# Optimization experiments

Measured on AMD Instinct MI355X. Metric: run time of the kernel, lower is better.

Reference implementation:

```python
import jax, jax.numpy as jnp
import numpy as np

TEMPERATURE = 8.0  # sqrt(d) with d = 64


def setup_inputs() -> dict:
    key = jax.random.key(0)
    kq, kk, kv, kmq, kmk = jax.random.split(key, 5)
    b, n, m, d, dv = 8, 4096, 4096, 64, 64
    return {
        "queries": jax.random.normal(kq, (b, n, d), dtype=jnp.float32),
        "keys": jax.random.normal(kk, (b, m, d), dtype=jnp.float32),
        "values": jax.random.normal(kv, (b, m, dv), dtype=jnp.float32),
        "mask_query": jax.random.randint(kmq, (b, n), 0, 2, dtype=jnp.int32),
        "mask_key": jax.random.randint(kmk, (b, m), 0, 2, dtype=jnp.int32),
    }


def reference(queries, keys, values, mask_query, mask_key):
    # scores: [b, n, m]
    attention = jnp.einsum("bnd,bmd->bnm", queries, keys)
    # multiplicative query mask: [b, n] -> [b, n, 1]
    attention = attention * mask_query[:, :, None].astype(queries.dtype)
    # additive log key mask: [b, m] -> [b, 1, m]; log(0) = -inf masks keys out
    attention = attention + jnp.log(mask_key[:, None, :].astype(queries.dtype))
    attention = jax.nn.softmax(attention / TEMPERATURE, axis=2)
    # output: [b, n, d']
    return jnp.einsum("bnm,bmv->bnv", attention, values)
```

## Files before the change

### kernel.cpp

```cpp
#include <hip/hip_runtime.h>


#define B_ 8
#define N_ 4096
#define M_ 4096
#define D_ 64

typedef __attribute__((ext_vector_type(8))) __bf16 bfrag;
typedef __attribute__((ext_vector_type(16))) float f32x16;
typedef __attribute__((ext_vector_type(4))) float f32x4;

union FragU { bfrag f; unsigned int u[4]; };

__device__ __forceinline__ unsigned int pkbf(float lo, float hi) {
  unsigned short a = __builtin_bit_cast(unsigned short, (__bf16)lo);
  unsigned short b = __builtin_bit_cast(unsigned short, (__bf16)hi);
  return ((unsigned int)b << 16) | (unsigned int)a;
}
__device__ __forceinline__ unsigned short bf1(float x) {
  return __builtin_bit_cast(unsigned short, (__bf16)x);
}

__global__ void attn_prepass(const float* __restrict__ kg, const float* __restrict__ vg,
                             char* __restrict__ kpack, char* __restrict__ vpack)
{
  const int bid = blockIdx.x, tid = threadIdx.x;
  if (bid < 1024) {
    const unsigned c0 = bid * 256 + tid;
    const int lane = c0 & 63;
    const unsigned u = c0 >> 6;
    const int f = u & 1, c = (u >> 1) & 3, tile = (u >> 3) & 63, batch = u >> 9;
    const int lq = lane & 31, lh = lane >> 5;
    const int row = tile * 64 + f * 32 + lq;
    const float* src = kg + (((size_t)batch * M_ + row) * D_ + c * 16 + lh * 8);
    float4 a = ((const float4*)src)[0], b = ((const float4*)src)[1];
    uint4 o;
    o.x = pkbf(a.x, a.y); o.y = pkbf(a.z, a.w);
    o.z = pkbf(b.x, b.y); o.w = pkbf(b.z, b.w);
    *(uint4*)(kpack + (size_t)c0 * 16) = o;
  } else {
    const unsigned c0 = (bid - 1024) * 256 + tid;
    const int lane = c0 & 63;
    const unsigned u = c0 >> 6;
    const int f = u & 1, mc = (u >> 1) & 3, tile = (u >> 3) & 63, batch = u >> 9;
    const int lq = lane & 31, lh = lane >> 5;
    const int key0 = tile * 64 + mc * 16 + lh * 8;
    const int dv = f * 32 + lq;
    const float* base = vg + (((size_t)batch * M_ + key0) * D_ + dv);
    unsigned short h[8];
#pragma unroll
    for (int j = 0; j < 8; ++j) h[j] = bf1(base[(size_t)j * D_]);
    uint4 o;
    o.x = (unsigned)h[0] | ((unsigned)h[1] << 16);
    o.y = (unsigned)h[2] | ((unsigned)h[3] << 16);
    o.z = (unsigned)h[4] | ((unsigned)h[5] << 16);
    o.w = (unsigned)h[6] | ((unsigned)h[7] << 16);
    *(uint4*)(vpack + (size_t)c0 * 16) = o;
  }
}

__global__ __launch_bounds__(256, 2) void attn_main(
    const float* __restrict__ qg, const int* __restrict__ mqg,
    const int* __restrict__ mkg, const char* __restrict__ kpack,
    const char* __restrict__ vpack, float* __restrict__ outg)
{
  __shared__ alignas(16) char smem[34048];
  const int tid  = threadIdx.x;
  const int lane = tid & 63;
  const int lq   = lane & 31;
  const int lh   = lane >> 5;
  const int wid  = tid >> 6;
  const int batch = blockIdx.x & 7;
  const int qbase = (blockIdx.x >> 3) * 64;

  float* lArrA = (float*)(smem + 32768);
  float* lArrB = (float*)(smem + 33280);
  float* IlvA  = (float*)(smem + 33792);
  float* IlvB  = (float*)(smem + 33920);

  {
    const int4* mk4 = (const int4*)(mkg + batch * M_);
    float* bl = (float*)smem;
#pragma unroll
    for (int j = 0; j < 4; ++j) {
      const int i4 = tid + j * 256;
      int4 m4 = mk4[i4];
      f32x4 bv;
      bv[0] = m4.x ? 0.f : -1e30f;
      bv[1] = m4.y ? 0.f : -1e30f;
      bv[2] = m4.z ? 0.f : -1e30f;
      bv[3] = m4.w ? 0.f : -1e30f;
      *(f32x4*)(bl + i4 * 4) = bv;
    }
  }

  bfrag qfA[4], qfB[4];
  {
    const int growA = qbase + lq;
    const float qsA = mqg[batch * N_ + growA] ? 0.1803368801111204f : 0.0f;
    const float* QpA = qg + ((size_t)batch * N_ + growA) * D_ + lh * 8;
#pragma unroll
    for (int c = 0; c < 4; ++c) {
      float4 a = *(const float4*)(QpA + c * 16);
      float4 b = *(const float4*)(QpA + c * 16 + 4);
      FragU f;
      f.u[0] = pkbf(a.x * qsA, a.y * qsA);
      f.u[1] = pkbf(a.z * qsA, a.w * qsA);
      f.u[2] = pkbf(b.x * qsA, b.y * qsA);
      f.u[3] = pkbf(b.z * qsA, b.w * qsA);
      qfA[c] = f.f;
    }
    const int growB = qbase + 32 + lq;
    const float qsB = mqg[batch * N_ + growB] ? 0.1803368801111204f : 0.0f;
    const float* QpB = qg + ((size_t)batch * N_ + growB) * D_ + lh * 8;
#pragma unroll
    for (int c = 0; c < 4; ++c) {
      float4 a = *(const float4*)(QpB + c * 16);
      float4 b = *(const float4*)(QpB + c * 16 + 4);
      FragU f;
      f.u[0] = pkbf(a.x * qsB, a.y * qsB);
      f.u[1] = pkbf(a.z * qsB, a.w * qsB);
      f.u[2] = pkbf(b.x * qsB, b.y * qsB);
      f.u[3] = pkbf(b.z * qsB, b.w * qsB);
      qfB[c] = f.f;
    }
  }
  __syncthreads();

  f32x16 oA0, oA1, oB0, oB1;
#pragma unroll
  for (int i = 0; i < 16; ++i) { oA0[i] = 0.f; oA1[i] = 0.f; oB0[i] = 0.f; oB1[i] = 0.f; }
  float lsumA = 0.f, lsumB = 0.f;

  const float* blw = (const float*)smem + wid * 1024;

  for (int t16 = 0; t16 < 16; ++t16) {
    const int tile = wid * 16 + t16;
    const size_t tb = (size_t)(batch * 64 + tile) * 8192 + (size_t)lane * 16;

    bfrag kf[4][2];
#pragma unroll
    for (int c = 0; c < 4; ++c) {
      kf[c][0] = *(const bfrag*)(kpack + tb + (c * 2 + 0) * 1024);
      kf[c][1] = *(const bfrag*)(kpack + tb + (c * 2 + 1) * 1024);
    }
    bfrag vf[4][2];
#pragma unroll
    for (int mc = 0; mc < 4; ++mc) {
      vf[mc][0] = *(const bfrag*)(vpack + tb + (mc * 2 + 0) * 1024);
      vf[mc][1] = *(const bfrag*)(vpack + tb + (mc * 2 + 1) * 1024);
    }

    f32x16 sA0, sA1, sB0, sB1;
#pragma unroll
    for (int i = 0; i < 16; ++i) { sA0[i] = 0.f; sA1[i] = 0.f; sB0[i] = 0.f; sB1[i] = 0.f; }
    __builtin_amdgcn_s_setprio(1);
#pragma unroll
    for (int c = 0; c < 4; ++c) {
      sA0 = __builtin_amdgcn_mfma_f32_32x32x16_bf16(kf[c][0], qfA[c], sA0, 0, 0, 0);
      sA1 = __builtin_amdgcn_mfma_f32_32x32x16_bf16(kf[c][1], qfA[c], sA1, 0, 0, 0);
      sB0 = __builtin_amdgcn_mfma_f32_32x32x16_bf16(kf[c][0], qfB[c], sB0, 0, 0, 0);
      sB1 = __builtin_amdgcn_mfma_f32_32x32x16_bf16(kf[c][1], qfB[c], sB1, 0, 0, 0);
    }
    __builtin_amdgcn_s_setprio(0);

    const float* bb = blw + t16 * 64;
    f32x4 psvA = {0.f, 0.f, 0.f, 0.f}, psvB = {0.f, 0.f, 0.f, 0.f};
#pragma unroll
    for (int g = 0; g < 4; ++g) {
      f32x4 b0 = *(const f32x4*)(bb + g * 8 + 4 * lh);
      f32x4 b1 = *(const f32x4*)(bb + 32 + g * 8 + 4 * lh);
#pragma unroll
      for (int r = 0; r < 4; ++r) {
        float pA0 = __builtin_amdgcn_exp2f(sA0[g * 4 + r] + b0[r]);
        float pA1 = __builtin_amdgcn_exp2f(sA1[g * 4 + r] + b1[r]);
        float pB0 = __builtin_amdgcn_exp2f(sB0[g * 4 + r] + b0[r]);
        float pB1 = __builtin_amdgcn_exp2f(sB1[g * 4 + r] + b1[r]);
        sA0[g * 4 + r] = pA0; sA1[g * 4 + r] = pA1;
        sB0[g * 4 + r] = pB0; sB1[g * 4 + r] = pB1;
        psvA[r] += pA0 + pA1;
        psvB[r] += pB0 + pB1;
      }
    }
    float psA = (psvA[0] + psvA[1]) + (psvA[2] + psvA[3]);
    float psB = (psvB[0] + psvB[1]) + (psvB[2] + psvB[3]);
    psA += __shfl_xor(psA, 32);
    psB += __shfl_xor(psB, 32);
    lsumA += psA;
    lsumB += psB;

#pragma unroll
    for (int mc = 0; mc < 4; ++mc) {
      unsigned int c01, c23, c45, c67;
      {
        const int Rb = (mc & 1) * 8;
        if (mc < 2) {
          c01 = pkbf(sA0[Rb + 0], sA0[Rb + 1]); c23 = pkbf(sA0[Rb + 2], sA0[Rb + 3]);
          c45 = pkbf(sA0[Rb + 4], sA0[Rb + 5]); c67 = pkbf(sA0[Rb + 6], sA0[Rb + 7]);
        } else {
          c01 = pkbf(sA1[Rb + 0], sA1[Rb + 1]); c23 = pkbf(sA1[Rb + 2], sA1[Rb + 3]);
          c45 = pkbf(sA1[Rb + 4], sA1[Rb + 5]); c67 = pkbf(sA1[Rb + 6], sA1[Rb + 7]);
        }
      }
      unsigned int t01 = (unsigned int)__shfl_xor((int)c01, 32);
      unsigned int t23 = (unsigned int)__shfl_xor((int)c23, 32);
      unsigned int t45 = (unsigned int)__shfl_xor((int)c45, 32);
      unsigned int t67 = (unsigned int)__shfl_xor((int)c67, 32);
      FragU pa;
      pa.u[0] = lh ? t45 : c01;
      pa.u[1] = lh ? t67 : c23;
      pa.u[2] = lh ? c45 : t01;
      pa.u[3] = lh ? c67 : t23;
      __builtin_amdgcn_s_setprio(1);
      oA0 = __builtin_amdgcn_mfma_f32_32x32x16_bf16(pa.f, vf[mc][0], oA0, 0, 0, 0);
      oA1 = __builtin_amdgcn_mfma_f32_32x32x16_bf16(pa.f, vf[mc][1], oA1, 0, 0, 0);
      __builtin_amdgcn_s_setprio(0);
    }
#pragma unroll
    for (int mc = 0; mc < 4; ++mc) {
      unsigned int c01, c23, c45, c67;
      {
        const int Rb = (mc & 1) * 8;
        if (mc < 2) {
          c01 = pkbf(sB0[Rb + 0], sB0[Rb + 1]); c23 = pkbf(sB0[Rb + 2], sB0[Rb + 3]);
          c45 = pkbf(sB0[Rb + 4], sB0[Rb + 5]); c67 = pkbf(sB0[Rb + 6], sB0[Rb + 7]);
        } else {
          c01 = pkbf(sB1[Rb + 0], sB1[Rb + 1]); c23 = pkbf(sB1[Rb + 2], sB1[Rb + 3]);
          c45 = pkbf(sB1[Rb + 4], sB1[Rb + 5]); c67 = pkbf(sB1[Rb + 6], sB1[Rb + 7]);
        }
      }
      unsigned int t01 = (unsigned int)__shfl_xor((int)c01, 32);
      unsigned int t23 = (unsigned int)__shfl_xor((int)c23, 32);
      unsigned int t45 = (unsigned int)__shfl_xor((int)c45, 32);
      unsigned int t67 = (unsigned int)__shfl_xor((int)c67, 32);
      FragU pa;
      pa.u[0] = lh ? t45 : c01;
      pa.u[1] = lh ? t67 : c23;
      pa.u[2] = lh ? c45 : t01;
      pa.u[3] = lh ? c67 : t23;
      __builtin_amdgcn_s_setprio(1);
      oB0 = __builtin_amdgcn_mfma_f32_32x32x16_bf16(pa.f, vf[mc][0], oB0, 0, 0, 0);
      oB1 = __builtin_amdgcn_mfma_f32_32x32x16_bf16(pa.f, vf[mc][1], oB1, 0, 0, 0);
      __builtin_amdgcn_s_setprio(0);
    }
  }

  if (lane < 32) { lArrA[wid * 32 + lane] = lsumA; lArrB[wid * 32 + lane] = lsumB; }
  __syncthreads();
  {
    float ltA = 0.f, ltB = 0.f;
#pragma unroll
    for (int w = 0; w < 4; ++w) { ltA += lArrA[w * 32 + lq]; ltB += lArrB[w * 32 + lq]; }
    if (wid == 0 && lane < 32) { IlvA[lane] = 1.f / ltA; IlvB[lane] = 1.f / ltB; }
  }
  __syncthreads();
#pragma unroll
  for (int g = 0; g < 4; ++g) {
    f32x4 IvA = *(const f32x4*)(IlvA + g * 8 + 4 * lh);
    f32x4 IvB = *(const f32x4*)(IlvB + g * 8 + 4 * lh);
#pragma unroll
    for (int rr = 0; rr < 4; ++rr) {
      oA0[g * 4 + rr] *= IvA[rr];
      oA1[g * 4 + rr] *= IvA[rr];
      oB0[g * 4 + rr] *= IvB[rr];
      oB1[g * 4 + rr] *= IvB[rr];
    }
  }
  float* bufsA = (float*)smem;
  float* bufsB = (float*)smem + 4096;
  float* dA = bufsA + (wid & 1) * 2048;
  float* dB = bufsB + (wid & 1) * 2048;
  if (wid < 2) {
#pragma unroll
    for (int r = 0; r < 16; ++r) {
      const int row = (r & 3) + 8 * (r >> 2) + 4 * lh;
      dA[row * 64 + lq]      = oA0[r];
      dA[row * 64 + 32 + lq] = oA1[r];
      dB[row * 64 + lq]      = oB0[r];
      dB[row * 64 + 32 + lq] = oB1[r];
    }
  }
  __syncthreads();
  if (wid >= 2) {
#pragma unroll
    for (int r = 0; r < 16; ++r) {
      const int row = (r & 3) + 8 * (r >> 2) + 4 * lh;
      dA[row * 64 + lq]      += oA0[r];
      dA[row * 64 + 32 + lq] += oA1[r];
      dB[row * 64 + lq]      += oB0[r];
      dB[row * 64 + 32 + lq] += oB1[r];
    }
  }
  __syncthreads();
  {
    float* op = outg + ((size_t)batch * N_ + qbase) * 64;
    const int i = tid * 8;
    f32x4 a0 = *(const f32x4*)(bufsA + i),     a1 = *(const f32x4*)(bufsA + 2048 + i);
    f32x4 b0 = *(const f32x4*)(bufsA + i + 4), b1 = *(const f32x4*)(bufsA + 2048 + i + 4);
#pragma unroll
    for (int r = 0; r < 4; ++r) { a0[r] += a1[r]; b0[r] += b1[r]; }
    *(f32x4*)(op + i)     = a0;
    *(f32x4*)(op + i + 4) = b0;
    f32x4 c0 = *(const f32x4*)(bufsB + i),     c1 = *(const f32x4*)(bufsB + 2048 + i);
    f32x4 d0 = *(const f32x4*)(bufsB + i + 4), d1 = *(const f32x4*)(bufsB + 2048 + i + 4);
#pragma unroll
    for (int r = 0; r < 4; ++r) { c0[r] += c1[r]; d0[r] += d1[r]; }
    *(f32x4*)(op + 2048 + i)     = c0;
    *(f32x4*)(op + 2048 + i + 4) = d0;
  }
}

__device__ __forceinline__ unsigned int swz(unsigned int byte) {
  return byte ^ (((byte >> 7) & 7) << 4);
}

__global__ __launch_bounds__(256, 2) void attn_fused(
    const float* __restrict__ qg, const float* __restrict__ kg,
    const float* __restrict__ vg, const int* __restrict__ mqg,
    const int* __restrict__ mkg, float* __restrict__ outg)
{
  __shared__ alignas(16) char smem[35072];
  const int tid  = threadIdx.x;
  const int lane = tid & 63;
  const int lq   = lane & 31;
  const int lh   = lane >> 5;
  const int wid  = tid >> 6;
  const int khalf = wid >> 1;
  const int qrw  = (wid & 1) * 32;
  const int batch = blockIdx.x & 7;
  const int qbase = (blockIdx.x >> 3) * 64;

  char* Kl = smem + khalf * 8192;
  char* Vl = smem + 16384 + khalf * 8192;
  float* kbf    = (float*)(smem + 32768);
  float* alphav = (float*)(smem + 33280);
  float* mM     = (float*)(smem + 33792);
  float* mL     = (float*)(smem + 34048);
  float* bC0    = (float*)(smem + 34304);
  float* bC1    = (float*)(smem + 34560);

  const int grow = qbase + qrw + lq;
  const float qs = mqg[batch * N_ + grow] ? 0.1803368801111204f : 0.0f;
  bfrag qf[4];
  {
    const float* Qp = qg + ((size_t)batch * N_ + grow) * D_ + lh * 8;
#pragma unroll
    for (int c = 0; c < 4; ++c) {
      float4 a = *(const float4*)(Qp + c * 16);
      float4 b = *(const float4*)(Qp + c * 16 + 4);
      FragU f;
      f.u[0] = pkbf(a.x * qs, a.y * qs);
      f.u[1] = pkbf(a.z * qs, a.w * qs);
      f.u[2] = pkbf(b.x * qs, b.y * qs);
      f.u[3] = pkbf(b.z * qs, b.w * qs);
      qf[c] = f.f;
    }
  }

  const int sid   = tid & 127;
  const int shalf = tid >> 7;

  f32x16 o0, o1;
#pragma unroll
  for (int i = 0; i < 16; ++i) { o0[i] = 0.f; o1[i] = 0.f; }
  float m2 = -1e30f, lsum = 0.f;

  for (int t = 0; t < 32; ++t) {
    __syncthreads();
    {
      const int kb0 = shalf * 2048 + t * 64;
      const float4* K4 = (const float4*)(kg + ((size_t)batch * M_ + kb0) * D_);
      const float4* V4 = (const float4*)(vg + ((size_t)batch * M_ + kb0) * D_);
      char* Ks = smem + shalf * 8192;
      char* Vs = smem + 16384 + shalf * 8192;
#pragma unroll
      for (int j = 0; j < 8; ++j) {
        int idx = sid + j * 128;
        float4 a = K4[idx];
        int row = idx >> 4, col = (idx & 15) << 2;
        *(uint2*)(Ks + swz((unsigned)(row * 128 + col * 2))) =
            make_uint2(pkbf(a.x, a.y), pkbf(a.z, a.w));
        float4 b = V4[idx];
        int vk = idx >> 4, vc = (idx & 15) << 2;
        *(unsigned short*)(Vs + swz((unsigned)((vc + 0) * 128 + vk * 2))) = bf1(b.x);
        *(unsigned short*)(Vs + swz((unsigned)((vc + 1) * 128 + vk * 2))) = bf1(b.y);
        *(unsigned short*)(Vs + swz((unsigned)((vc + 2) * 128 + vk * 2))) = bf1(b.z);
        *(unsigned short*)(Vs + swz((unsigned)((vc + 3) * 128 + vk * 2))) = bf1(b.w);
      }
      if (sid < 64)
        kbf[shalf * 64 + sid] = mkg[batch * M_ + kb0 + sid] ? 0.f : -1e30f;
    }
    __syncthreads();

    f32x16 s0, s1;
#pragma unroll
    for (int i = 0; i < 16; ++i) { s0[i] = 0.f; s1[i] = 0.f; }
#pragma unroll
    for (int c = 0; c < 4; ++c) {
      bfrag kf0 = *(const bfrag*)(Kl + swz((unsigned)(lq * 128 + (c * 16 + lh * 8) * 2)));
      bfrag kf1 = *(const bfrag*)(Kl + swz((unsigned)((32 + lq) * 128 + (c * 16 + lh * 8) * 2)));
      s0 = __builtin_amdgcn_mfma_f32_32x32x16_bf16(kf0, qf[c], s0, 0, 0, 0);
      s1 = __builtin_amdgcn_mfma_f32_32x32x16_bf16(kf1, qf[c], s1, 0, 0, 0);
    }

    const float* kbh = kbf + khalf * 64;
    float mx = -1e30f;
#pragma unroll
    for (int g = 0; g < 4; ++g) {
      f32x4 b0 = *(const f32x4*)(kbh + g * 8 + 4 * lh);
      f32x4 b1 = *(const f32x4*)(kbh + 32 + g * 8 + 4 * lh);
#pragma unroll
      for (int r = 0; r < 4; ++r) {
        s0[g * 4 + r] += b0[r];
        s1[g * 4 + r] += b1[r];
        mx = fmaxf(mx, fmaxf(s0[g * 4 + r], s1[g * 4 + r]));
      }
    }
    mx = fmaxf(mx, __shfl_xor(mx, 32));

    if (__any(mx > m2 + 8.f)) {
      float mn = fmaxf(m2, mx);
      float al = __builtin_amdgcn_exp2f(m2 - mn);
      if (lane < 32) alphav[wid * 32 + lane] = al;
      asm volatile("s_waitcnt lgkmcnt(0)" ::: "memory");
#pragma unroll
      for (int g = 0; g < 4; ++g) {
        f32x4 av = *(const f32x4*)(alphav + wid * 32 + g * 8 + 4 * lh);
#pragma unroll
        for (int r = 0; r < 4; ++r) { o0[g * 4 + r] *= av[r]; o1[g * 4 + r] *= av[r]; }
      }
      lsum *= al;
      m2 = mn;
    }

    float ps = 0.f;
#pragma unroll
    for (int i = 0; i < 16; ++i) {
      float p0 = __builtin_amdgcn_exp2f(s0[i] - m2);
      float p1 = __builtin_amdgcn_exp2f(s1[i] - m2);
      s0[i] = p0; s1[i] = p1;
      ps += p0 + p1;
    }
    ps += __shfl_xor(ps, 32);
    lsum += ps;

#pragma unroll
    for (int mc = 0; mc < 4; ++mc) {
      unsigned int c01, c23, c45, c67;
      {
        const int Rb = (mc & 1) * 8;
        if (mc < 2) {
          c01 = pkbf(s0[Rb + 0], s0[Rb + 1]); c23 = pkbf(s0[Rb + 2], s0[Rb + 3]);
          c45 = pkbf(s0[Rb + 4], s0[Rb + 5]); c67 = pkbf(s0[Rb + 6], s0[Rb + 7]);
        } else {
          c01 = pkbf(s1[Rb + 0], s1[Rb + 1]); c23 = pkbf(s1[Rb + 2], s1[Rb + 3]);
          c45 = pkbf(s1[Rb + 4], s1[Rb + 5]); c67 = pkbf(s1[Rb + 6], s1[Rb + 7]);
        }
      }
      unsigned int t01 = (unsigned int)__shfl_xor((int)c01, 32);
      unsigned int t23 = (unsigned int)__shfl_xor((int)c23, 32);
      unsigned int t45 = (unsigned int)__shfl_xor((int)c45, 32);
      unsigned int t67 = (unsigned int)__shfl_xor((int)c67, 32);
      FragU pa;
      pa.u[0] = lh ? t45 : c01;
      pa.u[1] = lh ? t67 : c23;
      pa.u[2] = lh ? c45 : t01;
      pa.u[3] = lh ? c67 : t23;
      bfrag vf0 = *(const bfrag*)(Vl + swz((unsigned)(lq * 128 + (mc * 16 + lh * 8) * 2)));
      bfrag vf1 = *(const bfrag*)(Vl + swz((unsigned)((32 + lq) * 128 + (mc * 16 + lh * 8) * 2)));
      o0 = __builtin_amdgcn_mfma_f32_32x32x16_bf16(pa.f, vf0, o0, 0, 0, 0);
      o1 = __builtin_amdgcn_mfma_f32_32x32x16_bf16(pa.f, vf1, o1, 0, 0, 0);
    }
  }

  __syncthreads();
  float* Omg = (float*)smem;
  if (khalf == 1) {
    const int w = wid & 1;
    if (lane < 32) { mM[w * 32 + lane] = m2; mL[w * 32 + lane] = lsum; }
#pragma unroll
    for (int r = 0; r < 16; ++r) {
      const int row = (r & 3) + 8 * (r >> 2) + 4 * lh;
      Omg[w * 2048 + row * 64 + lq]      = o0[r];
      Omg[w * 2048 + row * 64 + 32 + lq] = o1[r];
    }
  }
  __syncthreads();
  if (khalf == 0) {
    const int w = wid & 1;
    float m1 = mM[w * 32 + lq], l1 = mL[w * 32 + lq];
    float msf = fmaxf(m2, m1);
    float c0 = __builtin_amdgcn_exp2f(m2 - msf);
    float c1 = __builtin_amdgcn_exp2f(m1 - msf);
    float il = 1.f / (lsum * c0 + l1 * c1);
    if (lane < 32) { bC0[w * 32 + lane] = c0 * il; bC1[w * 32 + lane] = c1 * il; }
    asm volatile("s_waitcnt lgkmcnt(0)" ::: "memory");
    float* outp = outg + ((size_t)batch * N_ + qbase + qrw) * 64;
#pragma unroll
    for (int g = 0; g < 4; ++g) {
      f32x4 a0 = *(const f32x4*)(bC0 + w * 32 + g * 8 + 4 * lh);
      f32x4 a1 = *(const f32x4*)(bC1 + w * 32 + g * 8 + 4 * lh);
#pragma unroll
      for (int rr = 0; rr < 4; ++rr) {
        const int r = g * 4 + rr;
        const int row = rr + 8 * g + 4 * lh;
        float r0 = o0[r] * a0[rr] + Omg[w * 2048 + row * 64 + lq]      * a1[rr];
        float r1 = o1[r] * a0[rr] + Omg[w * 2048 + row * 64 + 32 + lq] * a1[rr];
        outp[(size_t)row * 64 + lq]      = r0;
        outp[(size_t)row * 64 + 32 + lq] = r1;
      }
    }
  }
}

extern "C" void kernel_launch(void* const* d_in, const int* in_sizes, int n_in,
                              void* d_out, int out_size, void* d_ws, size_t ws_size,
                              hipStream_t stream) {
  const float* q  = (const float*)d_in[0];
  const float* k  = (const float*)d_in[1];
  const float* v  = (const float*)d_in[2];
  const int*   mq = (const int*)d_in[3];
  const int*   mk = (const int*)d_in[4];
  float* out = (float*)d_out;

  const size_t kp_off = 0;
  const size_t vp_off = (size_t)B_ * 64 * 8192;
  const size_t need   = vp_off * 2;

  if (ws_size >= need) {
    char* kpack = (char*)d_ws + kp_off;
    char* vpack = (char*)d_ws + vp_off;
    attn_prepass<<<dim3(2048), dim3(256), 0, stream>>>(k, v, kpack, vpack);
    attn_main<<<dim3(512), dim3(256), 0, stream>>>(q, mq, mk, kpack, vpack, out);
  } else {
    attn_fused<<<dim3(512), dim3(256), 0, stream>>>(q, k, v, mq, mk, out);
  }
}
```

Baseline: 60.02 us.

## Permute key rows in prepack so P fragments need no cross-lane shuffles

Result: faster. 55.64 us (-7.3%).

```diff
diff --git a/kernel.cpp b/kernel.cpp
--- a/kernel.cpp
+++ b/kernel.cpp
@@ -31,7 +31,8 @@
     const unsigned u = c0 >> 6;
     const int f = u & 1, c = (u >> 1) & 3, tile = (u >> 3) & 63, batch = u >> 9;
     const int lq = lane & 31, lh = lane >> 5;
-    const int row = tile * 64 + f * 32 + lq;
+    const int lqp = (lq & 19) | ((lq & 4) << 1) | ((lq & 8) >> 1);
+    const int row = tile * 64 + f * 32 + lqp;
     const float* src = kg + (((size_t)batch * M_ + row) * D_ + c * 16 + lh * 8);
     float4 a = ((const float4*)src)[0], b = ((const float4*)src)[1];
     uint4 o;
@@ -84,7 +85,8 @@
 #pragma unroll
     for (int j = 0; j < 4; ++j) {
       const int i4 = tid + j * 256;
-      int4 m4 = mk4[i4];
+      const int i4s = (i4 & ~3) | ((i4 & 1) << 1) | ((i4 >> 1) & 1);
+      int4 m4 = mk4[i4s];
       f32x4 bv;
       bv[0] = m4.x ? 0.f : -1e30f;
       bv[1] = m4.y ? 0.f : -1e30f;
@@ -182,35 +184,24 @@
         psvB[r] += pB0 + pB1;
       }
     }
-    float psA = (psvA[0] + psvA[1]) + (psvA[2] + psvA[3]);
-    float psB = (psvB[0] + psvB[1]) + (psvB[2] + psvB[3]);
-    psA += __shfl_xor(psA, 32);
-    psB += __shfl_xor(psB, 32);
-    lsumA += psA;
-    lsumB += psB;
+    lsumA += (psvA[0] + psvA[1]) + (psvA[2] + psvA[3]);
+    lsumB += (psvB[0] + psvB[1]) + (psvB[2] + psvB[3]);
 
 #pragma unroll
     for (int mc = 0; mc < 4; ++mc) {
-      unsigned int c01, c23, c45, c67;
-      {
-        const int Rb = (mc & 1) * 8;
-        if (mc < 2) {
-          c01 = pkbf(sA0[Rb + 0], sA0[Rb + 1]); c23 = pkbf(sA0[Rb + 2], sA0[Rb + 3]);
-          c45 = pkbf(sA0[Rb + 4], sA0[Rb + 5]); c67 = pkbf(sA0[Rb + 6], sA0[Rb + 7]);
-        } else {
-          c01 = pkbf(sA1[Rb + 0], sA1[Rb + 1]); c23 = pkbf(sA1[Rb + 2], sA1[Rb + 3]);
-          c45 = pkbf(sA1[Rb + 4], sA1[Rb + 5]); c67 = pkbf(sA1[Rb + 6], sA1[Rb + 7]);
-        }
-      }
-      unsigned int t01 = (unsigned int)__shfl_xor((int)c01, 32);
-      unsigned int t23 = (unsigned int)__shfl_xor((int)c23, 32);
-      unsigned int t45 = (unsigned int)__shfl_xor((int)c45, 32);
-      unsigned int t67 = (unsigned int)__shfl_xor((int)c67, 32);
+      const int Rb = (mc & 1) * 8;
       FragU pa;
-      pa.u[0] = lh ? t45 : c01;
-      pa.u[1] = lh ? t67 : c23;
-      pa.u[2] = lh ? c45 : t01;
-      pa.u[3] = lh ? c67 : t23;
+      if (mc < 2) {
+        pa.u[0] = pkbf(sA0[Rb + 0], sA0[Rb + 1]);
+        pa.u[1] = pkbf(sA0[Rb + 2], sA0[Rb + 3]);
+        pa.u[2] = pkbf(sA0[Rb + 4], sA0[Rb + 5]);
+        pa.u[3] = pkbf(sA0[Rb + 6], sA0[Rb + 7]);
+      } else {
+        pa.u[0] = pkbf(sA1[Rb + 0], sA1[Rb + 1]);
+        pa.u[1] = pkbf(sA1[Rb + 2], sA1[Rb + 3]);
+        pa.u[2] = pkbf(sA1[Rb + 4], sA1[Rb + 5]);
+        pa.u[3] = pkbf(sA1[Rb + 6], sA1[Rb + 7]);
+      }
       __builtin_amdgcn_s_setprio(1);
       oA0 = __builtin_amdgcn_mfma_f32_32x32x16_bf16(pa.f, vf[mc][0], oA0, 0, 0, 0);
       oA1 = __builtin_amdgcn_mfma_f32_32x32x16_bf16(pa.f, vf[mc][1], oA1, 0, 0, 0);
@@ -218,32 +209,28 @@
     }
 #pragma unroll
     for (int mc = 0; mc < 4; ++mc) {
-      unsigned int c01, c23, c45, c67;
-      {
-        const int Rb = (mc & 1) * 8;
-        if (mc < 2) {
-          c01 = pkbf(sB0[Rb + 0], sB0[Rb + 1]); c23 = pkbf(sB0[Rb + 2], sB0[Rb + 3]);
-          c45 = pkbf(sB0[Rb + 4], sB0[Rb + 5]); c67 = pkbf(sB0[Rb + 6], sB0[Rb + 7]);
-        } else {
-          c01 = pkbf(sB1[Rb + 0], sB1[Rb + 1]); c23 = pkbf(sB1[Rb + 2], sB1[Rb + 3]);
-          c45 = pkbf(sB1[Rb + 4], sB1[Rb + 5]); c67 = pkbf(sB1[Rb + 6], sB1[Rb + 7]);
-        }
-      }
-      unsigned int t01 = (unsigned int)__shfl_xor((int)c01, 32);
-      unsigned int t23 = (unsigned int)__shfl_xor((int)c23, 32);
-      unsigned int t45 = (unsigned int)__shfl_xor((int)c45, 32);
-      unsigned int t67 = (unsigned int)__shfl_xor((int)c67, 32);
+      const int Rb = (mc & 1) * 8;
       FragU pa;
-      pa.u[0] = lh ? t45 : c01;
-      pa.u[1] = lh ? t67 : c23;
-      pa.u[2] = lh ? c45 : t01;
-      pa.u[3] = lh ? c67 : t23;
+      if (mc < 2) {
+        pa.u[0] = pkbf(sB0[Rb + 0], sB0[Rb + 1]);
+        pa.u[1] = pkbf(sB0[Rb + 2], sB0[Rb + 3]);
+        pa.u[2] = pkbf(sB0[Rb + 4], sB0[Rb + 5]);
+        pa.u[3] = pkbf(sB0[Rb + 6], sB0[Rb + 7]);
+      } else {
+        pa.u[0] = pkbf(sB1[Rb + 0], sB1[Rb + 1]);
+        pa.u[1] = pkbf(sB1[Rb + 2], sB1[Rb + 3]);
+        pa.u[2] = pkbf(sB1[Rb + 4], sB1[Rb + 5]);
+        pa.u[3] = pkbf(sB1[Rb + 6], sB1[Rb + 7]);
+      }
       __builtin_amdgcn_s_setprio(1);
       oB0 = __builtin_amdgcn_mfma_f32_32x32x16_bf16(pa.f, vf[mc][0], oB0, 0, 0, 0);
       oB1 = __builtin_amdgcn_mfma_f32_32x32x16_bf16(pa.f, vf[mc][1], oB1, 0, 0, 0);
       __builtin_amdgcn_s_setprio(0);
     }
   }
+
+  lsumA += __shfl_xor(lsumA, 32);
+  lsumB += __shfl_xor(lsumB, 32);
 
   if (lane < 32) { lArrA[wid * 32 + lane] = lsumA; lArrB[wid * 32 + lane] = lsumB; }
   __syncthreads();
```
